# Performance work log

Hardware: AMD Instinct MI355X
Metric: run time of the kernel (lower is better)

Reference implementation:

```python
import jax, jax.numpy as jnp
import numpy as np

HID = 256
BN_EPS = 1e-5
LN_EPS = 1e-5


def setup_inputs() -> dict:
    key = jax.random.key(0)
    ks = jax.random.split(key, 32)
    N, E, B = 50000, 400000, 2048
    F_ATOM, F_PROT = 70, 480

    def lin(k, fi, fo):
        return jax.random.normal(k, (fi, fo), jnp.float32) / np.sqrt(fi).astype(np.float32)

    inp = {
        "x": jax.random.normal(ks[0], (N, F_ATOM), jnp.float32),
        "edge_index": jax.random.randint(ks[1], (2, E), 0, N, jnp.int64),
        "batch": jnp.sort(jax.random.randint(ks[2], (N,), 0, B, jnp.int64)),
        "protein_emb": jax.random.normal(ks[3], (B, F_PROT), jnp.float32),
        # GIN layer 0 (70 -> 256)
        "gin0_w1": lin(ks[4], F_ATOM, HID), "gin0_b1": jnp.zeros((HID,), jnp.float32),
        "gin0_w2": lin(ks[5], HID, HID),    "gin0_b2": jnp.zeros((HID,), jnp.float32),
        "gin0_gamma": jnp.ones((HID,), jnp.float32), "gin0_beta": jnp.zeros((HID,), jnp.float32),
        # GIN layers 1..3 stacked (256 -> 256)
        "gin_w1": jnp.stack([lin(ks[6 + i], HID, HID) for i in range(3)]),
        "gin_b1": jnp.zeros((3, HID), jnp.float32),
        "gin_w2": jnp.stack([lin(ks[9 + i], HID, HID) for i in range(3)]),
        "gin_b2": jnp.zeros((3, HID), jnp.float32),
        "gin_gamma": jnp.ones((3, HID), jnp.float32),
        "gin_beta": jnp.zeros((3, HID), jnp.float32),
        # protein projector
        "wp": lin(ks[12], F_PROT, HID), "bp": jnp.zeros((HID,), jnp.float32),
        "ln_g": jnp.ones((HID,), jnp.float32), "ln_b": jnp.zeros((HID,), jnp.float32),
        # predictor MLP
        "wpr1": lin(ks[13], 2 * HID, 1024), "bpr1": jnp.zeros((1024,), jnp.float32),
        "wpr2": lin(ks[14], 1024, 512),     "bpr2": jnp.zeros((512,), jnp.float32),
        "wpr3": lin(ks[15], 512, 1),        "bpr3": jnp.zeros((1,), jnp.float32),
    }
    return inp


def _gin_layer(h, src, dst, n_nodes, w1, b1, w2, b2, gamma, beta):
    # GINConv (eps=0): mlp(x + sum_{j->i} x_j); scatter-add over destination
    agg = jax.ops.segment_sum(h[src], dst, num_segments=n_nodes)
    z = h + agg
    z = jax.nn.relu(z @ w1 + b1) @ w2 + b2
    # BatchNorm1d in eval mode: running_mean=0, running_var=1
    z = z * (gamma / np.sqrt(1.0 + BN_EPS).astype(np.float32)) + beta
    return jax.nn.relu(z)  # dropout is identity in eval


def reference(x, edge_index, batch, protein_emb,
              gin0_w1, gin0_b1, gin0_w2, gin0_b2, gin0_gamma, gin0_beta,
              gin_w1, gin_b1, gin_w2, gin_b2, gin_gamma, gin_beta,
              wp, bp, ln_g, ln_b,
              wpr1, bpr1, wpr2, bpr2, wpr3, bpr3):
    n_nodes = x.shape[0]
    n_graphs = protein_emb.shape[0]
    src, dst = edge_index[0], edge_index[1]

    h = _gin_layer(x, src, dst, n_nodes, gin0_w1, gin0_b1, gin0_w2, gin0_b2, gin0_gamma, gin0_beta)
    for i in range(3):  # layers 1..3 with residual
        h = h + _gin_layer(h, src, dst, n_nodes,
                           gin_w1[i], gin_b1[i], gin_w2[i], gin_b2[i], gin_gamma[i], gin_beta[i])

    # global_add_pool over graph ids
    drug_vec = jax.ops.segment_sum(h, batch, num_segments=n_graphs)  # [B, 256]

    # protein projector: Linear -> LayerNorm -> ReLU (dropout identity)
    p = protein_emb @ wp + bp
    mu = jnp.mean(p, axis=-1, keepdims=True)
    var = jnp.var(p, axis=-1, keepdims=True)
    p = (p - mu) * jax.lax.rsqrt(var + LN_EPS) * ln_g + ln_b
    prot_vec = jax.nn.relu(p)

    cat = jnp.concatenate([drug_vec, prot_vec], axis=1)  # [B, 512]
    h1 = jax.nn.relu(cat @ wpr1 + bpr1)
    h2 = jax.nn.relu(h1 @ wpr2 + bpr2)
    return h2 @ wpr3 + bpr3  # [B, 1]
```

## Files before the change

kernel.cpp:

```cpp
#include <hip/hip_runtime.h>

#define F_ATOM 70

#define FLAG_RELU 1
#define FLAG_BN   2
#define FLAG_RES  4

typedef __attribute__((ext_vector_type(8))) short short8;
typedef __attribute__((ext_vector_type(4))) float floatx4;

__device__ __forceinline__ float bf2f(unsigned short u) {
    union { unsigned int i; float f; } x; x.i = (unsigned int)u << 16; return x.f;
}
__device__ __forceinline__ unsigned short f2bf(float f) {
    union { float f; unsigned int i; } x; x.f = f;
    unsigned int r = x.i + 0x7fffu + ((x.i >> 16) & 1u);
    return (unsigned short)(r >> 16);
}
__device__ __forceinline__ float blo(unsigned int u){ union{unsigned int a; float f;}x; x.a=u<<16; return x.f; }
__device__ __forceinline__ float bhi(unsigned int u){ union{unsigned int a; float f;}x; x.a=u&0xffff0000u; return x.f; }


__global__ void count_kernel(const int* __restrict__ dst, int* __restrict__ cnt, int E) {
    int i = blockIdx.x * blockDim.x + threadIdx.x;
    if (i < E) atomicAdd(&cnt[dst[i]], 1);
}

__global__ void scan_kernel(const int* __restrict__ cnt, int* __restrict__ offs, int n) {
    __shared__ int wsum[16];
    __shared__ int carry_s;
    int t = threadIdx.x, lane = t & 63, wid = t >> 6;
    if (t == 0) carry_s = 0;
    __syncthreads();
    for (int base = 0; base < n; base += 1024) {
        int idx = base + t;
        int v = (idx < n) ? cnt[idx] : 0;
        int s = v;
        #pragma unroll
        for (int o = 1; o < 64; o <<= 1) {
            int x = __shfl_up(s, o);
            if (lane >= o) s += x;
        }
        if (lane == 63) wsum[wid] = s;
        __syncthreads();
        int woff = 0;
        #pragma unroll
        for (int wI = 0; wI < 16; ++wI) woff += (wI < wid) ? wsum[wI] : 0;
        int carry = carry_s;
        if (idx < n) offs[idx] = carry + woff + s - v;
        __syncthreads();
        if (t == 1023) carry_s = carry + woff + s;
        __syncthreads();
    }
    if (threadIdx.x == 0) offs[n] = carry_s;
}

__global__ void fill_kernel(const int* __restrict__ src, const int* __restrict__ dst,
                            const int* __restrict__ offs, int* __restrict__ cursor,
                            int* __restrict__ ssrc, int E) {
    int i = blockIdx.x * blockDim.x + threadIdx.x;
    if (i < E) {
        int d = dst[i];
        int pos = atomicAdd(&cursor[d], 1);
        ssrc[offs[d] + pos] = src[i];
    }
}

__global__ void graph_bounds_kernel(const int* __restrict__ batch, int* __restrict__ goffs,
                                    int N, int B) {
    int g = blockIdx.x * blockDim.x + threadIdx.x;
    if (g > B) return;
    int lo = 0, hi = N;
    while (lo < hi) {
        int mid = (lo + hi) >> 1;
        if (batch[mid] < g) lo = mid + 1; else hi = mid;
    }
    goffs[g] = lo;
}


__global__ void wtrans_kernel(const float* __restrict__ src, unsigned short* __restrict__ dst,
                              int K, int NC, int Kpad, int L) {
    int idx = blockIdx.x * blockDim.x + threadIdx.x;
    int per = NC * Kpad;
    if (idx >= per * L) return;
    int l = idx / per; int r2 = idx - l * per;
    int nrow = r2 / Kpad, k = r2 - nrow * Kpad;
    float v = (k < K) ? src[(size_t)l * K * NC + (size_t)k * NC + nrow] : 0.f;
    dst[idx] = f2bf(v);
}

__global__ void cvt_kernel(const float* __restrict__ src, unsigned short* __restrict__ dst, int n) {
    int i = blockIdx.x * blockDim.x + threadIdx.x;
    if (i < n) dst[i] = f2bf(src[i]);
}

__global__ void cvt_pad_kernel(const float* __restrict__ x, unsigned short* __restrict__ xb, int N) {
    long long idx = (long long)blockIdx.x * blockDim.x + threadIdx.x;
    if (idx >= (long long)N * 80) return;
    int node = (int)(idx / 80);
    int f = (int)(idx - (long long)node * 80);
    float v = (f < F_ATOM) ? x[(long long)node * F_ATOM + f] : 0.f;
    xb[idx] = f2bf(v);
}

__global__ __launch_bounds__(256) void agg0b_kernel(
    const unsigned short* __restrict__ xb, const int* __restrict__ offs,
    const int* __restrict__ ssrc, unsigned short* __restrict__ z0, int n) {
    int t = threadIdx.x;
    int node = blockIdx.x * 16 + (t >> 4);
    if (node >= n) return;
    int c = t & 15;
    if (c >= 10) {
        *(uint4*)(z0 + (size_t)node * 128 + c * 8) = make_uint4(0, 0, 0, 0);
        return;
    }
    const unsigned short* base = xb + (size_t)node * 80 + c * 8;
    uint4 v = *(const uint4*)base;
    float a[8];
    a[0]=blo(v.x); a[1]=bhi(v.x); a[2]=blo(v.y); a[3]=bhi(v.y);
    a[4]=blo(v.z); a[5]=bhi(v.z); a[6]=blo(v.w); a[7]=bhi(v.w);
    int s = offs[node], e2 = offs[node + 1];
    int k = s;
    for (; k + 3 < e2; k += 4) {
        uint4 u0 = *(const uint4*)(xb + (size_t)ssrc[k]     * 80 + c * 8);
        uint4 u1 = *(const uint4*)(xb + (size_t)ssrc[k + 1] * 80 + c * 8);
        uint4 u2 = *(const uint4*)(xb + (size_t)ssrc[k + 2] * 80 + c * 8);
        uint4 u3 = *(const uint4*)(xb + (size_t)ssrc[k + 3] * 80 + c * 8);
        a[0]+=blo(u0.x); a[1]+=bhi(u0.x); a[2]+=blo(u0.y); a[3]+=bhi(u0.y);
        a[4]+=blo(u0.z); a[5]+=bhi(u0.z); a[6]+=blo(u0.w); a[7]+=bhi(u0.w);
        a[0]+=blo(u1.x); a[1]+=bhi(u1.x); a[2]+=blo(u1.y); a[3]+=bhi(u1.y);
        a[4]+=blo(u1.z); a[5]+=bhi(u1.z); a[6]+=blo(u1.w); a[7]+=bhi(u1.w);
        a[0]+=blo(u2.x); a[1]+=bhi(u2.x); a[2]+=blo(u2.y); a[3]+=bhi(u2.y);
        a[4]+=blo(u2.z); a[5]+=bhi(u2.z); a[6]+=blo(u2.w); a[7]+=bhi(u2.w);
        a[0]+=blo(u3.x); a[1]+=bhi(u3.x); a[2]+=blo(u3.y); a[3]+=bhi(u3.y);
        a[4]+=blo(u3.z); a[5]+=bhi(u3.z); a[6]+=blo(u3.w); a[7]+=bhi(u3.w);
    }
    for (; k < e2; ++k) {
        uint4 u0 = *(const uint4*)(xb + (size_t)ssrc[k] * 80 + c * 8);
        a[0]+=blo(u0.x); a[1]+=bhi(u0.x); a[2]+=blo(u0.y); a[3]+=bhi(u0.y);
        a[4]+=blo(u0.z); a[5]+=bhi(u0.z); a[6]+=blo(u0.w); a[7]+=bhi(u0.w);
    }
    unsigned int o0 = (unsigned int)f2bf(a[0]) | ((unsigned int)f2bf(a[1]) << 16);
    unsigned int o1 = (unsigned int)f2bf(a[2]) | ((unsigned int)f2bf(a[3]) << 16);
    unsigned int o2 = (unsigned int)f2bf(a[4]) | ((unsigned int)f2bf(a[5]) << 16);
    unsigned int o3 = (unsigned int)f2bf(a[6]) | ((unsigned int)f2bf(a[7]) << 16);
    *(uint4*)(z0 + (size_t)node * 128 + c * 8) = make_uint4(o0, o1, o2, o3);
}

__global__ __launch_bounds__(256) void agg_bf16_kernel(
    const unsigned short* __restrict__ h, const int* __restrict__ offs,
    const int* __restrict__ ssrc, unsigned short* __restrict__ out, int n) {
    int t = threadIdx.x;
    int node = blockIdx.x * 8 + (t >> 5);
    if (node >= n) return;
    int f8 = (t & 31) * 8;
    uint4 v = *(const uint4*)(h + (size_t)node * 256 + f8);
    float a[8];
    a[0]=blo(v.x); a[1]=bhi(v.x); a[2]=blo(v.y); a[3]=bhi(v.y);
    a[4]=blo(v.z); a[5]=bhi(v.z); a[6]=blo(v.w); a[7]=bhi(v.w);
    int s = offs[node], e2 = offs[node + 1];
    int k = s;
    for (; k + 3 < e2; k += 4) {
        uint4 u0 = *(const uint4*)(h + (size_t)ssrc[k]     * 256 + f8);
        uint4 u1 = *(const uint4*)(h + (size_t)ssrc[k + 1] * 256 + f8);
        uint4 u2 = *(const uint4*)(h + (size_t)ssrc[k + 2] * 256 + f8);
        uint4 u3 = *(const uint4*)(h + (size_t)ssrc[k + 3] * 256 + f8);
        a[0]+=blo(u0.x); a[1]+=bhi(u0.x); a[2]+=blo(u0.y); a[3]+=bhi(u0.y);
        a[4]+=blo(u0.z); a[5]+=bhi(u0.z); a[6]+=blo(u0.w); a[7]+=bhi(u0.w);
        a[0]+=blo(u1.x); a[1]+=bhi(u1.x); a[2]+=blo(u1.y); a[3]+=bhi(u1.y);
        a[4]+=blo(u1.z); a[5]+=bhi(u1.z); a[6]+=blo(u1.w); a[7]+=bhi(u1.w);
        a[0]+=blo(u2.x); a[1]+=bhi(u2.x); a[2]+=blo(u2.y); a[3]+=bhi(u2.y);
        a[4]+=blo(u2.z); a[5]+=bhi(u2.z); a[6]+=blo(u2.w); a[7]+=bhi(u2.w);
        a[0]+=blo(u3.x); a[1]+=bhi(u3.x); a[2]+=blo(u3.y); a[3]+=bhi(u3.y);
        a[4]+=blo(u3.z); a[5]+=bhi(u3.z); a[6]+=blo(u3.w); a[7]+=bhi(u3.w);
    }
    for (; k < e2; ++k) {
        uint4 u0 = *(const uint4*)(h + (size_t)ssrc[k] * 256 + f8);
        a[0]+=blo(u0.x); a[1]+=bhi(u0.x); a[2]+=blo(u0.y); a[3]+=bhi(u0.y);
        a[4]+=blo(u0.z); a[5]+=bhi(u0.z); a[6]+=blo(u0.w); a[7]+=bhi(u0.w);
    }
    unsigned int o0 = (unsigned int)f2bf(a[0]) | ((unsigned int)f2bf(a[1]) << 16);
    unsigned int o1 = (unsigned int)f2bf(a[2]) | ((unsigned int)f2bf(a[3]) << 16);
    unsigned int o2 = (unsigned int)f2bf(a[4]) | ((unsigned int)f2bf(a[5]) << 16);
    unsigned int o3 = (unsigned int)f2bf(a[6]) | ((unsigned int)f2bf(a[7]) << 16);
    *(uint4*)(out + (size_t)node * 256 + f8) = make_uint4(o0, o1, o2, o3);
}


template<int KSH>
__global__ __launch_bounds__(512, 4) void fused_gin(
    const unsigned short* __restrict__ Z, const unsigned short* __restrict__ W1,
    const float* __restrict__ b1, const unsigned short* __restrict__ W2,
    const float* __restrict__ b2, const float* __restrict__ bng,
    const float* __restrict__ bnb, const unsigned short* __restrict__ res,
    unsigned short* __restrict__ out, int M)
{
    constexpr int CPR = KSH / 8;
    constexpr int NT1 = KSH / 32;
    __shared__ unsigned short sZ[128 * 256];
    const int T = threadIdx.x;
    const int lane = T & 63;
    const int w = T >> 6, wr = w >> 2, wc = w & 3;
    const int fr = lane & 15, hi = lane >> 4;
    const int crow = hi * 4;
    const int row0 = blockIdx.x * 128;

    #pragma unroll
    for (int i = 0; i < (128 * CPR) / 512; ++i) {
        int c = T + i * 512;
        int row = c / CPR, p = c % CPR;
        int pp = p ^ (row & 15);
        int gr = row0 + row; if (gr > M - 1) gr = M - 1;
        __builtin_amdgcn_global_load_lds(
            (const __attribute__((address_space(1))) void*)(Z + (size_t)gr * KSH + pp * 8),
            (__attribute__((address_space(3))) void*)&sZ[c * 8], 16, 0, 0);
    }
    __syncthreads();

    floatx4 acc[4][4];
    #pragma unroll
    for (int m = 0; m < 4; ++m)
        #pragma unroll
        for (int n = 0; n < 4; ++n)
            acc[m][n] = (floatx4){0.f, 0.f, 0.f, 0.f};

    {
        short8 cur[4], nxt[4];
        #pragma unroll
        for (int n = 0; n < 4; ++n)
            cur[n] = *(const short8*)(W1 + (size_t)(wc * 64 + n * 16 + fr) * KSH + hi * 8);
        #pragma unroll
        for (int kk = 0; kk < NT1; ++kk) {
            if (kk + 1 < NT1) {
                #pragma unroll
                for (int n = 0; n < 4; ++n)
                    nxt[n] = *(const short8*)(W1 + (size_t)(wc * 64 + n * 16 + fr) * KSH + (kk + 1) * 32 + hi * 8);
            }
            short8 af[4];
            #pragma unroll
            for (int m = 0; m < 4; ++m) {
                int r = wr * 64 + m * 16 + fr;
                int byte = r * (KSH * 2) + ((kk * 64 + hi * 16) ^ ((r & 15) << 4));
                af[m] = *(const short8*)((const char*)sZ + byte);
            }
            #pragma unroll
            for (int m = 0; m < 4; ++m)
                #pragma unroll
                for (int n = 0; n < 4; ++n)
                    acc[m][n] = __builtin_amdgcn_mfma_f32_16x16x32_bf16(af[m], cur[n], acc[m][n], 0, 0, 0);
            #pragma unroll
            for (int n = 0; n < 4; ++n) cur[n] = nxt[n];
        }
    }
    __syncthreads();

    #pragma unroll
    for (int n = 0; n < 4; ++n) {
        int col = wc * 64 + n * 16 + fr;
        float bb = b1[col];
        #pragma unroll
        for (int m = 0; m < 4; ++m) {
            #pragma unroll
            for (int j = 0; j < 4; ++j) {
                int r = wr * 64 + m * 16 + crow + j;
                float y = fmaxf(acc[m][n][j] + bb, 0.f);
                int byte = r * 512 + ((col * 2) ^ ((r & 15) << 4));
                *(unsigned short*)((char*)sZ + byte) = f2bf(y);
            }
        }
    }
    __syncthreads();

    #pragma unroll
    for (int m = 0; m < 4; ++m)
        #pragma unroll
        for (int n = 0; n < 4; ++n)
            acc[m][n] = (floatx4){0.f, 0.f, 0.f, 0.f};
    {
        short8 cur[4], nxt[4];
        #pragma unroll
        for (int n = 0; n < 4; ++n)
            cur[n] = *(const short8*)(W2 + (size_t)(wc * 64 + n * 16 + fr) * 256 + hi * 8);
        #pragma unroll
        for (int kk = 0; kk < 8; ++kk) {
            if (kk < 7) {
                #pragma unroll
                for (int n = 0; n < 4; ++n)
                    nxt[n] = *(const short8*)(W2 + (size_t)(wc * 64 + n * 16 + fr) * 256 + (kk + 1) * 32 + hi * 8);
            }
            short8 af[4];
            #pragma unroll
            for (int m = 0; m < 4; ++m) {
                int r = wr * 64 + m * 16 + fr;
                int byte = r * 512 + ((kk * 64 + hi * 16) ^ ((r & 15) << 4));
                af[m] = *(const short8*)((const char*)sZ + byte);
            }
            #pragma unroll
            for (int m = 0; m < 4; ++m)
                #pragma unroll
                for (int n = 0; n < 4; ++n)
                    acc[m][n] = __builtin_amdgcn_mfma_f32_16x16x32_bf16(af[m], cur[n], acc[m][n], 0, 0, 0);
            #pragma unroll
            for (int n = 0; n < 4; ++n) cur[n] = nxt[n];
        }
    }
    __syncthreads();

    {
        const float inv = rsqrtf(1.f + 1e-5f);
        #pragma unroll
        for (int n = 0; n < 4; ++n) {
            int col = wc * 64 + n * 16 + fr;
            float bb = b2[col];
            float sc = bng[col] * inv, be = bnb[col];
            #pragma unroll
            for (int m = 0; m < 4; ++m) {
                #pragma unroll
                for (int j = 0; j < 4; ++j) {
                    int r = wr * 64 + m * 16 + crow + j;
                    float y = (acc[m][n][j] + bb) * sc + be;
                    y = fmaxf(y, 0.f);
                    int byte = r * 512 + ((col * 2) ^ ((r & 15) << 4));
                    *(unsigned short*)((char*)sZ + byte) = f2bf(y);
                }
            }
        }
    }
    __syncthreads();

    #pragma unroll
    for (int i = 0; i < 8; ++i) {
        int c = T + i * 512;
        int row = c >> 5, slot = c & 31;
        int gr = row0 + row;
        if (gr >= M) continue;
        int byte = row * 512 + ((slot * 16) ^ ((row & 15) << 4));
        short8 v = *(const short8*)((const char*)sZ + byte);
        if (res) {
            short8 rv = *(const short8*)(res + (size_t)gr * 256 + slot * 8);
            #pragma unroll
            for (int e = 0; e < 8; ++e) {
                float f = bf2f((unsigned short)v[e]) + bf2f((unsigned short)rv[e]);
                v[e] = (short)f2bf(f);
            }
        }
        *(short8*)(out + (size_t)gr * 256 + slot * 8) = v;
    }
}


__global__ __launch_bounds__(256) void mfma_gemm(
    const unsigned short* __restrict__ A, const unsigned short* __restrict__ Bt,
    const float* __restrict__ bias, const float* __restrict__ bng,
    const float* __restrict__ bnb, const unsigned short* __restrict__ res,
    unsigned short* __restrict__ out, int M, int K, int NC, int flags)
{
    __shared__ unsigned short sA[2][128 * 32];
    __shared__ unsigned short sB[2][128 * 32];
    const int T = threadIdx.x;
    const int lane = T & 63;
    const int w = T >> 6, wr = w >> 1, wc = w & 1;
    const int row0 = blockIdx.x * 128;
    const int col0 = blockIdx.y * 128;
    const int nt = K >> 5;

    floatx4 acc[4][4];
    #pragma unroll
    for (int m = 0; m < 4; ++m)
        #pragma unroll
        for (int n = 0; n < 4; ++n)
            acc[m][n] = (floatx4){0.f, 0.f, 0.f, 0.f};

    auto stage = [&](int buf, int k0) {
        #pragma unroll
        for (int it = 0; it < 2; ++it) {
            int c = T + it * 256;
            int r = c >> 2, p = c & 3;
            int gr = row0 + r; if (gr > M - 1) gr = M - 1;
            const unsigned short* gA = A + (size_t)gr * K + k0 + p * 8;
            __builtin_amdgcn_global_load_lds(
                (const __attribute__((address_space(1))) void*)gA,
                (__attribute__((address_space(3))) void*)&sA[buf][c * 8], 16, 0, 0);
            const unsigned short* gB = Bt + (size_t)(col0 + r) * K + k0 + p * 8;
            __builtin_amdgcn_global_load_lds(
                (const __attribute__((address_space(1))) void*)gB,
                (__attribute__((address_space(3))) void*)&sB[buf][c * 8], 16, 0, 0);
        }
    };

    auto compute = [&](int buf) {
        const int fr = lane & 15;
        const int kh = (lane >> 4) * 8;
        short8 af[4], bv[4];
        #pragma unroll
        for (int m = 0; m < 4; ++m)
            af[m] = *(const short8*)&sA[buf][(wr * 64 + m * 16 + fr) * 32 + kh];
        #pragma unroll
        for (int n = 0; n < 4; ++n)
            bv[n] = *(const short8*)&sB[buf][(wc * 64 + n * 16 + fr) * 32 + kh];
        #pragma unroll
        for (int m = 0; m < 4; ++m)
            #pragma unroll
            for (int n = 0; n < 4; ++n)
                acc[m][n] = __builtin_amdgcn_mfma_f32_16x16x32_bf16(af[m], bv[n], acc[m][n], 0, 0, 0);
    };

    stage(0, 0);
    __syncthreads();
    int cur = 0;
    for (int t = 0; t < nt - 1; ++t) {
        stage(cur ^ 1, (t + 1) * 32);
        compute(cur);
        __syncthreads();
        cur ^= 1;
    }
    compute(cur);

    const int crow = (lane >> 4) * 4;
    const int ccol = lane & 15;
    const float inv = rsqrtf(1.f + 1e-5f);
    #pragma unroll
    for (int n = 0; n < 4; ++n) {
        int col = col0 + wc * 64 + n * 16 + ccol;
        float bb = bias ? bias[col] : 0.f;
        float sc = 1.f, be = 0.f;
        if (flags & FLAG_BN) { sc = bng[col] * inv; be = bnb[col]; }
        #pragma unroll
        for (int m = 0; m < 4; ++m) {
            #pragma unroll
            for (int j = 0; j < 4; ++j) {
                int r = row0 + wr * 64 + m * 16 + crow + j;
                if (r >= M) continue;
                float y = acc[m][n][j] + bb;
                if (flags & FLAG_BN) y = y * sc + be;
                if (flags & FLAG_RELU) y = fmaxf(y, 0.f);
                if (flags & FLAG_RES) y += bf2f(res[(size_t)r * NC + col]);
                out[(size_t)r * NC + col] = f2bf(y);
            }
        }
    }
}


__global__ void pool_kernel(const unsigned short* __restrict__ h, const int* __restrict__ goffs,
                            unsigned short* __restrict__ out, int ldout) {
    int g = blockIdx.x;
    int f = threadIdx.x;
    int s = goffs[g], e = goffs[g + 1];
    float acc = 0.f;
    for (int i = s; i < e; ++i) acc += bf2f(h[(size_t)i * 256 + f]);
    out[(size_t)g * ldout + f] = f2bf(acc);
}

__global__ void ln_relu_kernel(const unsigned short* __restrict__ p, const float* __restrict__ g,
                               const float* __restrict__ b, unsigned short* __restrict__ out, int ldout) {
    int row = blockIdx.x;
    int t = threadIdx.x;
    float v = bf2f(p[(size_t)row * 256 + t]);
    float s1 = v, s2 = v * v;
    #pragma unroll
    for (int o = 32; o > 0; o >>= 1) { s1 += __shfl_xor(s1, o); s2 += __shfl_xor(s2, o); }
    __shared__ float as1[4], as2[4];
    int w = t >> 6, lane = t & 63;
    if (lane == 0) { as1[w] = s1; as2[w] = s2; }
    __syncthreads();
    float tot1 = as1[0] + as1[1] + as1[2] + as1[3];
    float tot2 = as2[0] + as2[1] + as2[2] + as2[3];
    float mean = tot1 * (1.f / 256.f);
    float var = tot2 * (1.f / 256.f) - mean * mean;
    float y = (v - mean) * rsqrtf(var + 1e-5f) * g[t] + b[t];
    out[(size_t)row * ldout + t] = f2bf(fmaxf(y, 0.f));
}

__global__ void pred3_kernel(const unsigned short* __restrict__ h2, const float* __restrict__ w,
                             const float* __restrict__ b, float* __restrict__ out, int B) {
    int row = blockIdx.x * 4 + (threadIdx.x >> 6);
    int lane = threadIdx.x & 63;
    if (row >= B) return;
    float acc = 0.f;
    #pragma unroll
    for (int k = 0; k < 512; k += 64) acc += bf2f(h2[(size_t)row * 512 + k + lane]) * w[k + lane];
    #pragma unroll
    for (int o = 32; o > 0; o >>= 1) acc += __shfl_xor(acc, o);
    if (lane == 0) out[row] = acc + b[0];
}


extern "C" void kernel_launch(void* const* d_in, const int* in_sizes, int n_in,
                              void* d_out, int out_size, void* d_ws, size_t ws_size,
                              hipStream_t stream) {
    const float* x    = (const float*)d_in[0];
    const int*   ei   = (const int*)d_in[1];
    const int*   batch= (const int*)d_in[2];
    const float* pemb = (const float*)d_in[3];
    const float* g0w1 = (const float*)d_in[4];
    const float* g0b1 = (const float*)d_in[5];
    const float* g0w2 = (const float*)d_in[6];
    const float* g0b2 = (const float*)d_in[7];
    const float* g0g  = (const float*)d_in[8];
    const float* g0be = (const float*)d_in[9];
    const float* gw1  = (const float*)d_in[10];
    const float* gb1  = (const float*)d_in[11];
    const float* gw2  = (const float*)d_in[12];
    const float* gb2  = (const float*)d_in[13];
    const float* gg   = (const float*)d_in[14];
    const float* gbe  = (const float*)d_in[15];
    const float* wp   = (const float*)d_in[16];
    const float* bp   = (const float*)d_in[17];
    const float* lng  = (const float*)d_in[18];
    const float* lnb  = (const float*)d_in[19];
    const float* wpr1 = (const float*)d_in[20];
    const float* bpr1 = (const float*)d_in[21];
    const float* wpr2 = (const float*)d_in[22];
    const float* bpr2 = (const float*)d_in[23];
    const float* wpr3 = (const float*)d_in[24];
    const float* bpr3 = (const float*)d_in[25];

    int N = in_sizes[0] / F_ATOM;
    int E = in_sizes[1] / 2;
    int B = in_sizes[3] / 480;

    char* wsp = (char*)d_ws;
    auto carve = [&](size_t bytes) {
        void* p = (void*)wsp;
        wsp += (bytes + 255) & ~(size_t)255;
        return p;
    };
    int* offs   = (int*)carve((size_t)(N + 1) * 4);
    int* cursor = (int*)carve((size_t)N * 4);
    int* ssrc   = (int*)carve((size_t)E * 4);
    int* goffs  = (int*)carve((size_t)(B + 1) * 4);
    unsigned short* xb   = (unsigned short*)carve((size_t)N * 80 * 2);
    unsigned short* z0   = (unsigned short*)carve((size_t)N * 128 * 2);
    unsigned short* hbuf = (unsigned short*)carve((size_t)N * 256 * 2);
    unsigned short* tbuf = (unsigned short*)carve((size_t)N * 256 * 2);
    unsigned short* zbuf = (unsigned short*)carve((size_t)N * 256 * 2);
    unsigned short* pembbf = (unsigned short*)carve((size_t)B * 480 * 2);
    unsigned short* ptmp = (unsigned short*)carve((size_t)B * 256 * 2);
    unsigned short* cat  = (unsigned short*)carve((size_t)B * 512 * 2);
    unsigned short* h1   = (unsigned short*)carve((size_t)B * 1024 * 2);
    unsigned short* h2   = (unsigned short*)carve((size_t)B * 512 * 2);
    unsigned short* w10t = (unsigned short*)carve((size_t)256 * 128 * 2);
    unsigned short* w20t = (unsigned short*)carve((size_t)256 * 256 * 2);
    unsigned short* w1t  = (unsigned short*)carve((size_t)3 * 256 * 256 * 2);
    unsigned short* w2t  = (unsigned short*)carve((size_t)3 * 256 * 256 * 2);
    unsigned short* wpt  = (unsigned short*)carve((size_t)256 * 480 * 2);
    unsigned short* wpr1t= (unsigned short*)carve((size_t)1024 * 512 * 2);
    unsigned short* wpr2t= (unsigned short*)carve((size_t)512 * 1024 * 2);

    const int* srcp = ei;
    const int* dstp = ei + E;

    hipMemsetAsync(cursor, 0, (size_t)N * 4, stream);
    count_kernel<<<(E + 255) / 256, 256, 0, stream>>>(dstp, cursor, E);
    scan_kernel<<<1, 1024, 0, stream>>>(cursor, offs, N);
    hipMemsetAsync(cursor, 0, (size_t)N * 4, stream);
    fill_kernel<<<(E + 255) / 256, 256, 0, stream>>>(srcp, dstp, offs, cursor, ssrc, E);
    graph_bounds_kernel<<<(B + 256) / 256, 256, 0, stream>>>(batch, goffs, N, B);

    auto WT = [&](const float* s, unsigned short* d, int K, int NC, int Kpad, int L) {
        wtrans_kernel<<<(NC * Kpad * L + 255) / 256, 256, 0, stream>>>(s, d, K, NC, Kpad, L);
    };
    WT(g0w1, w10t, 70, 256, 128, 1);
    WT(g0w2, w20t, 256, 256, 256, 1);
    WT(gw1, w1t, 256, 256, 256, 3);
    WT(gw2, w2t, 256, 256, 256, 3);
    WT(wp, wpt, 480, 256, 480, 1);
    WT(wpr1, wpr1t, 512, 1024, 512, 1);
    WT(wpr2, wpr2t, 1024, 512, 1024, 1);
    cvt_kernel<<<(B * 480 + 255) / 256, 256, 0, stream>>>(pemb, pembbf, B * 480);
    cvt_pad_kernel<<<(int)(((long long)N * 80 + 255) / 256), 256, 0, stream>>>(x, xb, N);

    int rbN = (N + 127) / 128;

    agg0b_kernel<<<(N + 15) / 16, 256, 0, stream>>>(xb, offs, ssrc, z0, N);
    fused_gin<128><<<rbN, 512, 0, stream>>>(z0, w10t, g0b1, w20t, g0b2, g0g, g0be,
                                            nullptr, hbuf, N);

    unsigned short* H = hbuf; unsigned short* T2 = tbuf;
    for (int i = 0; i < 3; ++i) {
        agg_bf16_kernel<<<(N + 7) / 8, 256, 0, stream>>>(H, offs, ssrc, zbuf, N);
        fused_gin<256><<<rbN, 512, 0, stream>>>(zbuf, w1t + (size_t)i * 65536, gb1 + i * 256,
                                                w2t + (size_t)i * 65536, gb2 + i * 256,
                                                gg + i * 256, gbe + i * 256, H, T2, N);
        unsigned short* tmp = H; H = T2; T2 = tmp;
    }

    pool_kernel<<<B, 256, 0, stream>>>(H, goffs, cat, 512);

    mfma_gemm<<<dim3((B + 127) / 128, 2), 256, 0, stream>>>(pembbf, wpt, bp, nullptr, nullptr, nullptr,
                                                            ptmp, B, 480, 256, 0);
    ln_relu_kernel<<<B, 256, 0, stream>>>(ptmp, lng, lnb, cat + 256, 512);

    mfma_gemm<<<dim3((B + 127) / 128, 8), 256, 0, stream>>>(cat, wpr1t, bpr1, nullptr, nullptr, nullptr,
                                                            h1, B, 512, 1024, FLAG_RELU);
    mfma_gemm<<<dim3((B + 127) / 128, 4), 256, 0, stream>>>(h1, wpr2t, bpr2, nullptr, nullptr, nullptr,
                                                            h2, B, 1024, 512, FLAG_RELU);
    pred3_kernel<<<(B + 3) / 4, 256, 0, stream>>>(h2, wpr3, bpr3, (float*)d_out, B);
}
```

Before: 573.2 us.

## Merge prep conversions into one kernel and halve fused GIN row tile

Replaces the nine separate weight-transpose and conversion launches with a single grid-stride prep kernel that dispatches on a flat index range, cutting launch count. The fused GIN kernel now uses 64-row tiles with 256 threads (4 waves, one row group) instead of 128 rows with 512 threads, halving LDS per block and doubling the block count. This aims at higher occupancy and better tail balance across CUs, at the cost of each wave reloading the W1/W2 fragments for fewer rows, so there is less weight reuse per block.

```diff
diff --git a/kernel.cpp b/kernel.cpp
--- a/kernel.cpp
+++ b/kernel.cpp
@@ -79,29 +79,77 @@
 }
 
 
-__global__ void wtrans_kernel(const float* __restrict__ src, unsigned short* __restrict__ dst,
-                              int K, int NC, int Kpad, int L) {
-    int idx = blockIdx.x * blockDim.x + threadIdx.x;
-    int per = NC * Kpad;
-    if (idx >= per * L) return;
-    int l = idx / per; int r2 = idx - l * per;
-    int nrow = r2 / Kpad, k = r2 - nrow * Kpad;
-    float v = (k < K) ? src[(size_t)l * K * NC + (size_t)k * NC + nrow] : 0.f;
-    dst[idx] = f2bf(v);
-}
-
-__global__ void cvt_kernel(const float* __restrict__ src, unsigned short* __restrict__ dst, int n) {
-    int i = blockIdx.x * blockDim.x + threadIdx.x;
-    if (i < n) dst[i] = f2bf(src[i]);
-}
-
-__global__ void cvt_pad_kernel(const float* __restrict__ x, unsigned short* __restrict__ xb, int N) {
-    long long idx = (long long)blockIdx.x * blockDim.x + threadIdx.x;
-    if (idx >= (long long)N * 80) return;
-    int node = (int)(idx / 80);
-    int f = (int)(idx - (long long)node * 80);
-    float v = (f < F_ATOM) ? x[(long long)node * F_ATOM + f] : 0.f;
-    xb[idx] = f2bf(v);
+__global__ __launch_bounds__(256) void prep_kernel(
+    const float* __restrict__ x, const float* __restrict__ pemb,
+    const float* __restrict__ g0w1, const float* __restrict__ g0w2,
+    const float* __restrict__ gw1, const float* __restrict__ gw2,
+    const float* __restrict__ wp, const float* __restrict__ wpr1, const float* __restrict__ wpr2,
+    unsigned short* __restrict__ xb, unsigned short* __restrict__ pembbf,
+    unsigned short* __restrict__ w10t, unsigned short* __restrict__ w20t,
+    unsigned short* __restrict__ w1t, unsigned short* __restrict__ w2t,
+    unsigned short* __restrict__ wpt, unsigned short* __restrict__ wpr1t,
+    unsigned short* __restrict__ wpr2t, int N, int B)
+{
+    const long long sz0 = (long long)N * 80;
+    const long long sz1 = (long long)B * 480;
+    const long long szw10 = 256 * 128, szw20 = 256 * 256;
+    const long long szw1 = 3 * 256 * 256, szw2 = 3 * 256 * 256;
+    const long long szwp = 256 * 480, szp1 = 1024 * 512, szp2 = 512 * 1024;
+    const long long total = sz0 + sz1 + szw10 + szw20 + szw1 + szw2 + szwp + szp1 + szp2;
+    const long long stride = (long long)gridDim.x * blockDim.x;
+    for (long long idx = (long long)blockIdx.x * blockDim.x + threadIdx.x; idx < total; idx += stride) {
+        long long r = idx;
+        if (r < sz0) {
+            int node = (int)(r / 80), f = (int)(r - (long long)node * 80);
+            xb[r] = f2bf(f < F_ATOM ? x[(long long)node * F_ATOM + f] : 0.f);
+            continue;
+        }
+        r -= sz0;
+        if (r < sz1) { pembbf[r] = f2bf(pemb[r]); continue; }
+        r -= sz1;
+        if (r < szw10) {
+            int nr = (int)(r >> 7), k = (int)(r & 127);
+            w10t[r] = f2bf(k < F_ATOM ? g0w1[k * 256 + nr] : 0.f);
+            continue;
+        }
+        r -= szw10;
+        if (r < szw20) {
+            int nr = (int)(r >> 8), k = (int)(r & 255);
+            w20t[r] = f2bf(g0w2[k * 256 + nr]);
+            continue;
+        }
+        r -= szw20;
+        if (r < szw1) {
+            int l = (int)(r >> 16); int r2 = (int)(r & 65535);
+            int nr = r2 >> 8, k = r2 & 255;
+            w1t[r] = f2bf(gw1[(size_t)l * 65536 + k * 256 + nr]);
+            continue;
+        }
+        r -= szw1;
+        if (r < szw2) {
+            int l = (int)(r >> 16); int r2 = (int)(r & 65535);
+            int nr = r2 >> 8, k = r2 & 255;
+            w2t[r] = f2bf(gw2[(size_t)l * 65536 + k * 256 + nr]);
+            continue;
+        }
+        r -= szw2;
+        if (r < szwp) {
+            int nr = (int)(r / 480), k = (int)(r - (long long)nr * 480);
+            wpt[r] = f2bf(wp[k * 256 + nr]);
+            continue;
+        }
+        r -= szwp;
+        if (r < szp1) {
+            int nr = (int)(r >> 9), k = (int)(r & 511);
+            wpr1t[r] = f2bf(wpr1[k * 1024 + nr]);
+            continue;
+        }
+        r -= szp1;
+        {
+            int nr = (int)(r >> 10), k = (int)(r & 1023);
+            wpr2t[r] = f2bf(wpr2[k * 512 + nr]);
+        }
+    }
 }
 
 __global__ __launch_bounds__(256) void agg0b_kernel(
@@ -189,7 +237,7 @@
 
 
 template<int KSH>
-__global__ __launch_bounds__(512, 4) void fused_gin(
+__global__ __launch_bounds__(256, 4) void fused_gin(
     const unsigned short* __restrict__ Z, const unsigned short* __restrict__ W1,
     const float* __restrict__ b1, const unsigned short* __restrict__ W2,
     const float* __restrict__ b2, const float* __restrict__ bng,
@@ -198,17 +246,17 @@
 {
     constexpr int CPR = KSH / 8;
     constexpr int NT1 = KSH / 32;
-    __shared__ unsigned short sZ[128 * 256];
+    __shared__ unsigned short sZ[64 * 256];
     const int T = threadIdx.x;
     const int lane = T & 63;
-    const int w = T >> 6, wr = w >> 2, wc = w & 3;
+    const int wc = T >> 6;
     const int fr = lane & 15, hi = lane >> 4;
     const int crow = hi * 4;
-    const int row0 = blockIdx.x * 128;
-
-    #pragma unroll
-    for (int i = 0; i < (128 * CPR) / 512; ++i) {
-        int c = T + i * 512;
+    const int row0 = blockIdx.x * 64;
+
+    #pragma unroll
+    for (int i = 0; i < (64 * CPR) / 256; ++i) {
+        int c = T + i * 256;
         int row = c / CPR, p = c % CPR;
         int pp = p ^ (row & 15);
         int gr = row0 + row; if (gr > M - 1) gr = M - 1;
@@ -240,7 +288,7 @@
             short8 af[4];
             #pragma unroll
             for (int m = 0; m < 4; ++m) {
-                int r = wr * 64 + m * 16 + fr;
+                int r = m * 16 + fr;
                 int byte = r * (KSH * 2) + ((kk * 64 + hi * 16) ^ ((r & 15) << 4));
                 af[m] = *(const short8*)((const char*)sZ + byte);
             }
@@ -263,7 +311,7 @@
         for (int m = 0; m < 4; ++m) {
             #pragma unroll
             for (int j = 0; j < 4; ++j) {
-                int r = wr * 64 + m * 16 + crow + j;
+                int r = m * 16 + crow + j;
                 float y = fmaxf(acc[m][n][j] + bb, 0.f);
                 int byte = r * 512 + ((col * 2) ^ ((r & 15) << 4));
                 *(unsigned short*)((char*)sZ + byte) = f2bf(y);
@@ -292,7 +340,7 @@
             short8 af[4];
             #pragma unroll
             for (int m = 0; m < 4; ++m) {
-                int r = wr * 64 + m * 16 + fr;
+                int r = m * 16 + fr;
                 int byte = r * 512 + ((kk * 64 + hi * 16) ^ ((r & 15) << 4));
                 af[m] = *(const short8*)((const char*)sZ + byte);
             }
@@ -318,7 +366,7 @@
             for (int m = 0; m < 4; ++m) {
                 #pragma unroll
                 for (int j = 0; j < 4; ++j) {
-                    int r = wr * 64 + m * 16 + crow + j;
+                    int r = m * 16 + crow + j;
                     float y = (acc[m][n][j] + bb) * sc + be;
                     y = fmaxf(y, 0.f);
                     int byte = r * 512 + ((col * 2) ^ ((r & 15) << 4));
@@ -331,7 +379,7 @@
 
     #pragma unroll
     for (int i = 0; i < 8; ++i) {
-        int c = T + i * 512;
+        int c = T + i * 256;
         int row = c >> 5, slot = c & 31;
         int gr = row0 + row;
         if (gr >= M) continue;
@@ -559,29 +607,20 @@
     fill_kernel<<<(E + 255) / 256, 256, 0, stream>>>(srcp, dstp, offs, cursor, ssrc, E);
     graph_bounds_kernel<<<(B + 256) / 256, 256, 0, stream>>>(batch, goffs, N, B);
 
-    auto WT = [&](const float* s, unsigned short* d, int K, int NC, int Kpad, int L) {
-        wtrans_kernel<<<(NC * Kpad * L + 255) / 256, 256, 0, stream>>>(s, d, K, NC, Kpad, L);
-    };
-    WT(g0w1, w10t, 70, 256, 128, 1);
-    WT(g0w2, w20t, 256, 256, 256, 1);
-    WT(gw1, w1t, 256, 256, 256, 3);
-    WT(gw2, w2t, 256, 256, 256, 3);
-    WT(wp, wpt, 480, 256, 480, 1);
-    WT(wpr1, wpr1t, 512, 1024, 512, 1);
-    WT(wpr2, wpr2t, 1024, 512, 1024, 1);
-    cvt_kernel<<<(B * 480 + 255) / 256, 256, 0, stream>>>(pemb, pembbf, B * 480);
-    cvt_pad_kernel<<<(int)(((long long)N * 80 + 255) / 256), 256, 0, stream>>>(x, xb, N);
-
-    int rbN = (N + 127) / 128;
+    prep_kernel<<<2048, 256, 0, stream>>>(x, pemb, g0w1, g0w2, gw1, gw2, wp, wpr1, wpr2,
+                                          xb, pembbf, w10t, w20t, w1t, w2t, wpt, wpr1t, wpr2t,
+                                          N, B);
+
+    int rbN = (N + 63) / 64;
 
     agg0b_kernel<<<(N + 15) / 16, 256, 0, stream>>>(xb, offs, ssrc, z0, N);
-    fused_gin<128><<<rbN, 512, 0, stream>>>(z0, w10t, g0b1, w20t, g0b2, g0g, g0be,
+    fused_gin<128><<<rbN, 256, 0, stream>>>(z0, w10t, g0b1, w20t, g0b2, g0g, g0be,
                                             nullptr, hbuf, N);
 
     unsigned short* H = hbuf; unsigned short* T2 = tbuf;
     for (int i = 0; i < 3; ++i) {
         agg_bf16_kernel<<<(N + 7) / 8, 256, 0, stream>>>(H, offs, ssrc, zbuf, N);
-        fused_gin<256><<<rbN, 512, 0, stream>>>(zbuf, w1t + (size_t)i * 65536, gb1 + i * 256,
+        fused_gin<256><<<rbN, 256, 0, stream>>>(zbuf, w1t + (size_t)i * 65536, gb1 + i * 256,
                                                 w2t + (size_t)i * 65536, gb2 + i * 256,
                                                 gg + i * 256, gbe + i * 256, H, T2, N);
         unsigned short* tmp = H; H = T2; T2 = tmp;
```

Measured after the change: 557.2 us. 1.03x faster.
